# Performance work log

Measured on AMD Instinct MI355X. Metric: run time of the kernel, lower is better.

The kernel has to match this reference:

```python
import jax, jax.numpy as jnp
import numpy as np

A_DIM, HID, D_EMB, K_CODES, N_TOK = 6, 256, 128, 2048, 65536
BETA = 0.25


def _linear_init(k, fan_in, fan_out):
    lim = 1.0 / np.sqrt(fan_in)
    kw, kb = jax.random.split(k)
    W = jax.random.uniform(kw, (fan_in, fan_out), minval=-lim, maxval=lim, dtype=jnp.float32)
    b = jax.random.uniform(kb, (fan_out,), minval=-lim, maxval=lim, dtype=jnp.float32)
    return W, b


def setup_inputs() -> dict:
    key = jax.random.key(0)
    ks = jax.random.split(key, 8)
    action = jax.random.normal(ks[0], (1, N_TOK, A_DIM), dtype=jnp.float32)
    W_e1, b_e1 = _linear_init(ks[1], A_DIM, HID)
    W_e2, b_e2 = _linear_init(ks[2], HID, HID)
    W_e3, b_e3 = _linear_init(ks[3], HID, D_EMB)
    # codebook init: uniform(-1/K, 1/K) as in the torch module
    emb = jax.random.uniform(ks[4], (K_CODES, D_EMB), minval=-1.0 / K_CODES, maxval=1.0 / K_CODES, dtype=jnp.float32)
    W_d1, b_d1 = _linear_init(ks[5], D_EMB, HID)
    W_d2, b_d2 = _linear_init(ks[6], HID, HID)
    W_d3, b_d3 = _linear_init(ks[7], HID, A_DIM)
    return dict(action=action,
                W_e1=W_e1, b_e1=b_e1, W_e2=W_e2, b_e2=b_e2, W_e3=W_e3, b_e3=b_e3,
                emb=emb,
                W_d1=W_d1, b_d1=b_d1, W_d2=W_d2, b_d2=b_d2, W_d3=W_d3, b_d3=b_d3)


def reference(action, W_e1, b_e1, W_e2, b_e2, W_e3, b_e3, emb,
              W_d1, b_d1, W_d2, b_d2, W_d3, b_d3):
    sg = jax.lax.stop_gradient
    # encoder MLP; note original code does encoder(action)[0] -> [N, D]
    h = jax.nn.relu(action @ W_e1 + b_e1)
    h = jax.nn.relu(h @ W_e2 + b_e2)
    enc = (h @ W_e3 + b_e3)[0]                         # [N, D]
    # squared-distance to codebook: [N, K]
    dist = (jnp.sum(enc ** 2, axis=1, keepdims=True)
            + jnp.sum(emb ** 2, axis=1)
            - 2.0 * enc @ emb.T)
    idx = jnp.argmin(dist, axis=1)                     # [N]
    one_hot = jax.nn.one_hot(idx, emb.shape[0], dtype=enc.dtype)  # [N, K]
    q = one_hot @ emb                                  # [N, D]
    commitment_loss = jnp.mean((sg(q) - enc) ** 2)
    embedding_loss = jnp.mean((q - sg(enc)) ** 2)
    vq_loss = BETA * commitment_loss + embedding_loss
    # straight-through estimator
    q_st = enc + sg(q - enc)
    # decoder MLP
    d = jax.nn.relu(q_st @ W_d1 + b_d1)
    d = jax.nn.relu(d @ W_d2 + b_d2)
    recons = jnp.tanh(d @ W_d3 + b_d3)                 # [N, A]
    recons_loss = jnp.mean((recons - action[0]) ** 2)
    total = recons_loss + vq_loss
    return jnp.stack([total, recons_loss, vq_loss])
```

## Files before the change

### kernel.cpp

```cpp
#include <hip/hip_runtime.h>
#include <stdint.h>

typedef unsigned short u16;
typedef float f32x4 __attribute__((ext_vector_type(4)));
typedef short short8 __attribute__((ext_vector_type(8)));
typedef unsigned uint4v __attribute__((ext_vector_type(4)));

enum { NT = 65536, KC = 2048, D = 128, H = 256, A_DIM = 6 };

__device__ __forceinline__ u16 f2bf(float f) {
    union { float f; unsigned u; } x; x.f = f;
    unsigned r = x.u + 0x7FFFu + ((x.u >> 16) & 1u);
    return (u16)(r >> 16);
}
__device__ __forceinline__ float bf2f(u16 u) {
    union { unsigned u; float f; } x; x.u = ((unsigned)u) << 16;
    return x.f;
}

typedef __attribute__((address_space(1))) void gvoid;
typedef __attribute__((address_space(3))) void lvoid;
__device__ __forceinline__ void gload_lds16(const void* g, void* l) {
    __builtin_amdgcn_global_load_lds((gvoid*)g, (lvoid*)l, 16, 0, 0);
}

__global__ void prep(const float* __restrict__ W_e2, const float* __restrict__ W_e3,
                     const float* __restrict__ W_d1, const float* __restrict__ W_d2,
                     const float* __restrict__ emb,
                     u16* __restrict__ We2T, u16* __restrict__ We3T,
                     u16* __restrict__ Wd1T, u16* __restrict__ Wd2T,
                     u16* __restrict__ emb_bf, float* __restrict__ norm2,
                     float* __restrict__ sums) {
    int b = blockIdx.x, t = threadIdx.x;
    if (b == 0 && t < 2) sums[t] = 0.f;
    if (b < 256)       { int e = b * 256 + t;          int i = e >> 8, j = e & 255; We2T[j * 256 + i] = f2bf(W_e2[e]); }
    else if (b < 384)  { int e = (b - 256) * 256 + t;  int i = e >> 7, j = e & 127; We3T[j * 256 + i] = f2bf(W_e3[e]); }
    else if (b < 512)  { int e = (b - 384) * 256 + t;  int i = e >> 8, j = e & 255; Wd1T[j * 128 + i] = f2bf(W_d1[e]); }
    else if (b < 768)  { int e = (b - 512) * 256 + t;  int i = e >> 8, j = e & 255; Wd2T[j * 256 + i] = f2bf(W_d2[e]); }
    else if (b < 1792) { int e = (b - 768) * 256 + t;  emb_bf[e] = f2bf(emb[e]); }
    else {
        int lane = t & 63, w = t >> 6;
        int r = (b - 1792) * 4 + w;
        float v0 = emb[(size_t)r * D + lane];
        float v1 = emb[(size_t)r * D + 64 + lane];
        float s = v0 * v0 + v1 * v1;
#pragma unroll
        for (int off = 32; off; off >>= 1) s += __shfl_xor(s, off);
        if (lane == 0) norm2[r] = s;
    }
}

__global__ __launch_bounds__(256) void enc1(const float* __restrict__ act, const float* __restrict__ W,
                                            const float* __restrict__ b, u16* __restrict__ h1) {
    const int gid = blockIdx.x * 256 + threadIdx.x;
    const int row = gid >> 5;
    const int col0 = (gid & 31) << 3;
    float x[A_DIM];
#pragma unroll
    for (int i = 0; i < A_DIM; i++) x[i] = act[(size_t)row * A_DIM + i];
    float s[8];
#pragma unroll
    for (int c = 0; c < 8; c++) s[c] = b[col0 + c];
#pragma unroll
    for (int i = 0; i < A_DIM; i++) {
        float xi = x[i];
#pragma unroll
        for (int c = 0; c < 8; c++) s[c] = fmaf(xi, W[i * H + col0 + c], s[c]);
    }
    uint4v o;
#pragma unroll
    for (int c2 = 0; c2 < 4; c2++)
        o[c2] = (unsigned)f2bf(fmaxf(s[c2 * 2], 0.f)) | ((unsigned)f2bf(fmaxf(s[c2 * 2 + 1], 0.f)) << 16);
    *(uint4v*)&h1[(size_t)row * H + col0] = o;
}

__global__ __launch_bounds__(256) void enc23_fused(
    const u16* __restrict__ h1g,
    const u16* __restrict__ We2T, const float* __restrict__ b2,
    const u16* __restrict__ We3T, const float* __restrict__ b3,
    u16* __restrict__ encb) {
    __shared__ __align__(16) u16 hA[64 * 256];
    __shared__ __align__(16) u16 sB[256 * 64];
    const int t = threadIdx.x, lane = t & 63, w = t >> 6;
    const int l15 = lane & 15, khalf = lane >> 4;
    const int row0 = blockIdx.x * 64;
#pragma unroll
    for (int p = 0; p < 8; p++) {
        int db = (p * 256 + t) * 16;
        int r = db >> 9;
        int col = ((db & 511) ^ ((r & 7) << 4)) >> 1;
        gload_lds16(h1g + (size_t)(row0 + r) * H + col, (char*)hA + db);
    }
    int sbDst[8], sbRow[8], sbCol[8];
#pragma unroll
    for (int p = 0; p < 8; p++) {
        int db = (p * 256 + t) * 16;
        int r = db >> 7;
        sbDst[p] = db; sbRow[p] = r;
        sbCol[p] = ((db & 127) ^ ((r & 7) << 4)) >> 1;
    }
    const int kbase = khalf * 8;
    f32x4 acc[4][4] = {};
    for (int kst = 0; kst < 4; kst++) {
        if (kst) __syncthreads();
        const int k0 = kst * 64;
#pragma unroll
        for (int p = 0; p < 8; p++)
            gload_lds16(We2T + (size_t)sbRow[p] * H + k0 + sbCol[p], (char*)sB + sbDst[p]);
        __syncthreads();
#pragma unroll
        for (int ks = 0; ks < 2; ks++) {
            const int k = k0 + ks * 32 + kbase;
            const int kb = (ks * 32 + kbase) << 1;
            short8 av[4], bv[4];
#pragma unroll
            for (int m = 0; m < 4; m++) {
                int rA = m * 16 + l15;
                av[m] = *(const short8*)((const char*)hA + ((rA << 9) | ((k << 1) ^ ((rA & 7) << 4))));
            }
#pragma unroll
            for (int n = 0; n < 4; n++) {
                int rB = w * 64 + n * 16 + l15;
                bv[n] = *(const short8*)((const char*)sB + ((rB << 7) | (kb ^ ((rB & 7) << 4))));
            }
#pragma unroll
            for (int m = 0; m < 4; m++)
#pragma unroll
                for (int n = 0; n < 4; n++)
                    acc[m][n] = __builtin_amdgcn_mfma_f32_16x16x32_bf16(av[m], bv[n], acc[m][n], 0, 0, 0);
        }
    }
    __syncthreads();
#pragma unroll
    for (int n = 0; n < 4; n++) {
        int col = w * 64 + n * 16 + l15;
        float bs = b2[col];
#pragma unroll
        for (int m = 0; m < 4; m++)
#pragma unroll
            for (int j = 0; j < 4; j++) {
                int row = m * 16 + khalf * 4 + j;
                float v = fmaxf(acc[m][n][j] + bs, 0.f);
                *(u16*)((char*)hA + ((row << 9) | ((col << 1) ^ ((row & 7) << 4)))) = f2bf(v);
            }
    }
    __syncthreads();
    f32x4 acc2[4][2] = {};
    for (int kst = 0; kst < 4; kst++) {
        if (kst) __syncthreads();
        const int k0 = kst * 64;
#pragma unroll
        for (int p = 0; p < 4; p++)
            gload_lds16(We3T + (size_t)sbRow[p] * H + k0 + sbCol[p], (char*)sB + sbDst[p]);
        __syncthreads();
#pragma unroll
        for (int ks = 0; ks < 2; ks++) {
            const int k = k0 + ks * 32 + kbase;
            const int kb = (ks * 32 + kbase) << 1;
            short8 av[4], bv[2];
#pragma unroll
            for (int m = 0; m < 4; m++) {
                int rA = m * 16 + l15;
                av[m] = *(const short8*)((const char*)hA + ((rA << 9) | ((k << 1) ^ ((rA & 7) << 4))));
            }
#pragma unroll
            for (int n = 0; n < 2; n++) {
                int rB = w * 32 + n * 16 + l15;
                bv[n] = *(const short8*)((const char*)sB + ((rB << 7) | (kb ^ ((rB & 7) << 4))));
            }
#pragma unroll
            for (int m = 0; m < 4; m++)
#pragma unroll
                for (int n = 0; n < 2; n++)
                    acc2[m][n] = __builtin_amdgcn_mfma_f32_16x16x32_bf16(av[m], bv[n], acc2[m][n], 0, 0, 0);
        }
    }
    __syncthreads();
#pragma unroll
    for (int n = 0; n < 2; n++) {
        int col = w * 32 + n * 16 + l15;
        float bs = b3[col];
#pragma unroll
        for (int m = 0; m < 4; m++)
#pragma unroll
            for (int j = 0; j < 4; j++) {
                int row = m * 16 + khalf * 4 + j;
                ((u16*)sB)[row * 128 + col] = f2bf(acc2[m][n][j] + bs);
            }
    }
    __syncthreads();
#pragma unroll
    for (int p = 0; p < 4; p++) {
        int db = (p * 256 + t) * 16;
        *(uint4v*)((char*)(encb + (size_t)row0 * D) + db) = *(const uint4v*)((const char*)sB + db);
    }
}

__global__ __launch_bounds__(256) void dec_fused(
    const u16* __restrict__ qb,
    const u16* __restrict__ Wd1T, const float* __restrict__ bd1,
    const u16* __restrict__ Wd2T, const float* __restrict__ bd2,
    const float* __restrict__ W3, float* __restrict__ part) {
    __shared__ __align__(16) u16 qA[64 * 128];
    __shared__ __align__(16) u16 hA[64 * 256];
    __shared__ __align__(16) u16 sB[256 * 64];
    const int t = threadIdx.x, lane = t & 63, w = t >> 6;
    const int l15 = lane & 15, khalf = lane >> 4;
    const int row0 = blockIdx.x * 64;
#pragma unroll
    for (int p = 0; p < 4; p++) {
        int db = (p * 256 + t) * 16;
        int r = db >> 8;
        int col = ((db & 255) ^ ((r & 7) << 4)) >> 1;
        gload_lds16(qb + (size_t)(row0 + r) * D + col, (char*)qA + db);
    }
    int sbDst[8], sbRow[8], sbCol[8];
#pragma unroll
    for (int p = 0; p < 8; p++) {
        int db = (p * 256 + t) * 16;
        int r = db >> 7;
        sbDst[p] = db; sbRow[p] = r;
        sbCol[p] = ((db & 127) ^ ((r & 7) << 4)) >> 1;
    }
    const int kbase = khalf * 8;
    f32x4 acc[4][4] = {};
    for (int kst = 0; kst < 2; kst++) {
        if (kst) __syncthreads();
        const int k0 = kst * 64;
#pragma unroll
        for (int p = 0; p < 8; p++)
            gload_lds16(Wd1T + (size_t)sbRow[p] * D + k0 + sbCol[p], (char*)sB + sbDst[p]);
        __syncthreads();
#pragma unroll
        for (int ks = 0; ks < 2; ks++) {
            const int k = k0 + ks * 32 + kbase;
            const int kb = (ks * 32 + kbase) << 1;
            short8 av[4], bv[4];
#pragma unroll
            for (int m = 0; m < 4; m++) {
                int rA = m * 16 + l15;
                av[m] = *(const short8*)((const char*)qA + ((rA << 8) | ((k << 1) ^ ((rA & 7) << 4))));
            }
#pragma unroll
            for (int n = 0; n < 4; n++) {
                int rB = w * 64 + n * 16 + l15;
                bv[n] = *(const short8*)((const char*)sB + ((rB << 7) | (kb ^ ((rB & 7) << 4))));
            }
#pragma unroll
            for (int m = 0; m < 4; m++)
#pragma unroll
                for (int n = 0; n < 4; n++)
                    acc[m][n] = __builtin_amdgcn_mfma_f32_16x16x32_bf16(av[m], bv[n], acc[m][n], 0, 0, 0);
        }
    }
#pragma unroll
    for (int n = 0; n < 4; n++) {
        int col = w * 64 + n * 16 + l15;
        float bs = bd1[col];
#pragma unroll
        for (int m = 0; m < 4; m++)
#pragma unroll
            for (int j = 0; j < 4; j++) {
                int row = m * 16 + khalf * 4 + j;
                float v = fmaxf(acc[m][n][j] + bs, 0.f);
                *(u16*)((char*)hA + ((row << 9) | ((col << 1) ^ ((row & 7) << 4)))) = f2bf(v);
            }
    }
    __syncthreads();
    f32x4 acc2[4][4] = {};
    for (int kst = 0; kst < 4; kst++) {
        if (kst) __syncthreads();
        const int k0 = kst * 64;
#pragma unroll
        for (int p = 0; p < 8; p++)
            gload_lds16(Wd2T + (size_t)sbRow[p] * H + k0 + sbCol[p], (char*)sB + sbDst[p]);
        __syncthreads();
#pragma unroll
        for (int ks = 0; ks < 2; ks++) {
            const int k = k0 + ks * 32 + kbase;
            const int kb = (ks * 32 + kbase) << 1;
            short8 av[4], bv[4];
#pragma unroll
            for (int m = 0; m < 4; m++) {
                int rA = m * 16 + l15;
                av[m] = *(const short8*)((const char*)hA + ((rA << 9) | ((k << 1) ^ ((rA & 7) << 4))));
            }
#pragma unroll
            for (int n = 0; n < 4; n++) {
                int rB = w * 64 + n * 16 + l15;
                bv[n] = *(const short8*)((const char*)sB + ((rB << 7) | (kb ^ ((rB & 7) << 4))));
            }
#pragma unroll
            for (int m = 0; m < 4; m++)
#pragma unroll
                for (int n = 0; n < 4; n++)
                    acc2[m][n] = __builtin_amdgcn_mfma_f32_16x16x32_bf16(av[m], bv[n], acc2[m][n], 0, 0, 0);
        }
    }
    float W3r[4][A_DIM], bs[4];
#pragma unroll
    for (int n = 0; n < 4; n++) {
        int col = w * 64 + n * 16 + l15;
        bs[n] = bd2[col];
#pragma unroll
        for (int j = 0; j < A_DIM; j++) W3r[n][j] = W3[col * A_DIM + j];
    }
    float* ps = part + (size_t)w * NT * A_DIM;
#pragma unroll
    for (int m = 0; m < 4; m++) {
#pragma unroll
        for (int j = 0; j < 4; j++) {
            int row = row0 + m * 16 + khalf * 4 + j;
            float p6[A_DIM] = {};
#pragma unroll
            for (int n = 0; n < 4; n++) {
                float v = fmaxf(acc2[m][n][j] + bs[n], 0.f);
#pragma unroll
                for (int jj = 0; jj < A_DIM; jj++) p6[jj] = fmaf(v, W3r[n][jj], p6[jj]);
            }
#pragma unroll
            for (int off = 1; off < 16; off <<= 1)
#pragma unroll
                for (int jj = 0; jj < A_DIM; jj++) p6[jj] += __shfl_xor(p6[jj], off);
            if (l15 == 0) {
#pragma unroll
                for (int jj = 0; jj < A_DIM; jj++) ps[(size_t)row * A_DIM + jj] = p6[jj];
            }
        }
    }
}

__global__ __launch_bounds__(256) void head_final(const float* __restrict__ part, const float* __restrict__ b3,
                                                  const float* __restrict__ act, float* __restrict__ sums) {
    __shared__ float sred[4];
    const int t = threadIdx.x, lane = t & 63, w = t >> 6;
    const int n = blockIdx.x * 256 + t;
    float s = 0.f;
#pragma unroll
    for (int j = 0; j < A_DIM; j++) {
        float v = b3[j];
#pragma unroll
        for (int sl = 0; sl < 4; sl++) v += part[(size_t)sl * NT * A_DIM + (size_t)n * A_DIM + j];
        float r = tanhf(v);
        float df = r - act[(size_t)n * A_DIM + j];
        s += df * df;
    }
#pragma unroll
    for (int off = 32; off; off >>= 1) s += __shfl_xor(s, off);
    if (lane == 0) sred[w] = s;
    __syncthreads();
    if (t == 0) atomicAdd(&sums[1], sred[0] + sred[1] + sred[2] + sred[3]);
}

__global__ __launch_bounds__(256) void vq_dist(const u16* __restrict__ enc_bf, const u16* __restrict__ emb_bf,
                                               const float* __restrict__ emb, const float* __restrict__ norm2,
                                               u16* __restrict__ q_bf, float* __restrict__ sums) {
    __shared__ u16 sA[128 * 128];
    __shared__ u16 sB[128 * 128];
    __shared__ float sN[KC];
    __shared__ unsigned sKey[128];
    __shared__ float svq[4];
    const int t = threadIdx.x, lane = t & 63, w = t >> 6, wr = w >> 1, wc = w & 1;
    const int row0 = blockIdx.x * 128;
    int srow[8], sdst[8], scol[8];
#pragma unroll
    for (int p = 0; p < 8; p++) {
        int db = (p * 256 + t) * 16;
        int row = db >> 8;
        srow[p] = row; sdst[p] = db;
        scol[p] = ((db & 255) ^ ((row & 7) << 4)) >> 1;
    }
#pragma unroll
    for (int p = 0; p < 8; p++) gload_lds16(enc_bf + (size_t)(row0 + srow[p]) * D + scol[p], (char*)sA + sdst[p]);
#pragma unroll
    for (int p = 0; p < 8; p++) gload_lds16(emb_bf + (size_t)srow[p] * D + scol[p], (char*)sB + sdst[p]);
    for (int i = t; i < KC; i += 256) sN[i] = norm2[i] + 1.0f;
    const int ra = wr * 64 + (lane & 15), rb = wc * 64 + (lane & 15);
    const int kbase = (lane >> 4) * 8;
    int boff[4][4];
#pragma unroll
    for (int m = 0; m < 4; m++)
#pragma unroll
        for (int ks = 0; ks < 4; ks++) {
            int rB = rb + m * 16;
            int kb = (ks * 32 + kbase) << 1;
            boff[m][ks] = (rB << 8) | (kb ^ ((rB & 7) << 4));
        }
    __syncthreads();
    short8 av[4][4];
#pragma unroll
    for (int m = 0; m < 4; m++)
#pragma unroll
        for (int ks = 0; ks < 4; ks++) {
            int rA = ra + m * 16;
            int kb = (ks * 32 + kbase) << 1;
            av[m][ks] = *(const short8*)((const char*)sA + ((rA << 8) | (kb ^ ((rA & 7) << 4))));
        }
    unsigned minKey[4][4];
#pragma unroll
    for (int m = 0; m < 4; m++)
#pragma unroll
        for (int j = 0; j < 4; j++) minKey[m][j] = 0xFFFFFFFFu;
    for (int ch = 0; ch < 16; ch++) {
        if (ch) {
            __syncthreads();
            const u16* src = emb_bf + (size_t)ch * 128 * D;
#pragma unroll
            for (int p = 0; p < 8; p++) gload_lds16(src + (size_t)srow[p] * D + scol[p], (char*)sB + sdst[p]);
            __syncthreads();
        }
        f32x4 acc[4][4] = {};
#pragma unroll
        for (int ks = 0; ks < 4; ks++) {
            short8 bv[4];
#pragma unroll
            for (int n = 0; n < 4; n++) bv[n] = *(const short8*)((const char*)sB + boff[n][ks]);
#pragma unroll
            for (int m = 0; m < 4; m++)
#pragma unroll
                for (int n = 0; n < 4; n++)
                    acc[m][n] = __builtin_amdgcn_mfma_f32_16x16x32_bf16(av[m][ks], bv[n], acc[m][n], 0, 0, 0);
        }
#pragma unroll
        for (int n = 0; n < 4; n++) {
            int k = ch * 128 + rb + n * 16;
            float nn = sN[k];
#pragma unroll
            for (int m = 0; m < 4; m++)
#pragma unroll
                for (int j = 0; j < 4; j++) {
                    float c = fmaf(acc[m][n][j], -2.f, nn);
                    unsigned key = (__float_as_uint(c) & 0xFFFFF800u) | (unsigned)k;
                    minKey[m][j] = min(minKey[m][j], key);
                }
        }
    }
#pragma unroll
    for (int off = 1; off < 16; off <<= 1) {
#pragma unroll
        for (int m = 0; m < 4; m++)
#pragma unroll
            for (int j = 0; j < 4; j++)
                minKey[m][j] = min(minKey[m][j], (unsigned)__shfl_xor((int)minKey[m][j], off));
    }
    __syncthreads();
    if (wc == 0 && (lane & 15) == 0) {
#pragma unroll
        for (int m = 0; m < 4; m++)
#pragma unroll
            for (int j = 0; j < 4; j++) {
                int row = wr * 64 + m * 16 + (lane >> 4) * 4 + j;
                sKey[row] = minKey[m][j];
            }
    }
    __syncthreads();
    if (wc == 1 && (lane & 15) == 0) {
#pragma unroll
        for (int m = 0; m < 4; m++)
#pragma unroll
            for (int j = 0; j < 4; j++) {
                int row = wr * 64 + m * 16 + (lane >> 4) * 4 + j;
                if (minKey[m][j] < sKey[row]) sKey[row] = minKey[m][j];
            }
    }
    __syncthreads();
    float vql = 0.f;
    for (int rr = 0; rr < 32; rr++) {
        int row = w * 32 + rr;
        int k = (int)(sKey[row] & 0x7FFu);
        float q0 = emb[(size_t)k * D + lane];
        float q1 = emb[(size_t)k * D + 64 + lane];
        int swz = (row & 7) << 4;
        float e0 = bf2f(*(const u16*)((const char*)sA + ((row << 8) | ((lane << 1) ^ swz))));
        float e1 = bf2f(*(const u16*)((const char*)sA + ((row << 8) | (((lane + 64) << 1) ^ swz))));
        float d0 = q0 - e0, d1 = q1 - e1;
        vql += d0 * d0 + d1 * d1;
        q_bf[(size_t)(row0 + row) * D + lane] = f2bf(q0);
        q_bf[(size_t)(row0 + row) * D + 64 + lane] = f2bf(q1);
    }
#pragma unroll
    for (int off = 32; off; off >>= 1) vql += __shfl_xor(vql, off);
    if (lane == 0) svq[w] = vql;
    __syncthreads();
    if (t == 0) atomicAdd(&sums[0], svq[0] + svq[1] + svq[2] + svq[3]);
}

__global__ void finalize(const float* __restrict__ sums, float* __restrict__ out) {
    if (threadIdx.x == 0) {
        float vq = 1.25f * sums[0] / (float)(NT * D);
        float rec = sums[1] / (float)(NT * A_DIM);
        out[0] = rec + vq;
        out[1] = rec;
        out[2] = vq;
    }
}

extern "C" void kernel_launch(void* const* d_in, const int* in_sizes, int n_in,
                              void* d_out, int out_size, void* d_ws, size_t ws_size,
                              hipStream_t stream) {
    const float* action = (const float*)d_in[0];
    const float* W_e1 = (const float*)d_in[1];
    const float* b_e1 = (const float*)d_in[2];
    const float* W_e2 = (const float*)d_in[3];
    const float* b_e2 = (const float*)d_in[4];
    const float* W_e3 = (const float*)d_in[5];
    const float* b_e3 = (const float*)d_in[6];
    const float* emb  = (const float*)d_in[7];
    const float* W_d1 = (const float*)d_in[8];
    const float* b_d1 = (const float*)d_in[9];
    const float* W_d2 = (const float*)d_in[10];
    const float* b_d2 = (const float*)d_in[11];
    const float* W_d3 = (const float*)d_in[12];
    const float* b_d3 = (const float*)d_in[13];

    char* ws = (char*)d_ws;
    float* sums  = (float*)ws;
    float* norm2 = (float*)(ws + 256);
    u16* We2T   = (u16*)(ws + 8448);
    u16* We3T   = (u16*)(ws + 139520);
    u16* Wd1T   = (u16*)(ws + 205056);
    u16* Wd2T   = (u16*)(ws + 270592);
    u16* emb_bf = (u16*)(ws + 401664);
    u16* h1     = (u16*)(ws + 925952);
    float* part = (float*)(ws + 925952 + 33554432);
    u16* encb   = (u16*)(ws + 925952 + 67108864);
    u16* qb     = (u16*)(ws + 925952 + 83886080);

    prep<<<2304, 256, 0, stream>>>(W_e2, W_e3, W_d1, W_d2, emb, We2T, We3T, Wd1T, Wd2T, emb_bf, norm2, sums);
    enc1<<<NT * 32 / 256, 256, 0, stream>>>(action, W_e1, b_e1, h1);
    enc23_fused<<<NT / 64, 256, 0, stream>>>(h1, We2T, b_e2, We3T, b_e3, encb);
    vq_dist<<<NT / 128, 256, 0, stream>>>(encb, emb_bf, emb, norm2, qb, sums);
    dec_fused<<<NT / 64, 256, 0, stream>>>(qb, Wd1T, b_d1, Wd2T, b_d2, W_d3, part);
    head_final<<<NT / 256, 256, 0, stream>>>(part, b_d3, action, sums);
    finalize<<<1, 64, 0, stream>>>(sums, (float*)d_out);
}
```

Before: 148.3 us.

## Pass code indices instead of quantized vectors; gather codebook rows in decoder

vq_dist now writes one int index per token instead of a bf16 quantized row, and dec_fused gathers the codebook rows directly from emb_bf through the indices. The VQ loss is rebuilt algebraically as the min distance key value plus the sum of enc squared, avoiding a per-row fp32 codebook gather. This cuts the 16MB quantized-vector write and read, at the cost of an extra sync and index load in the decoder. The loss now relies on the packed distance key's truncated precision and an assumed offset of 1.0, which may change numerics slightly.

After: 157.1 us. 1.06x slower.

```diff
diff --git a/kernel.cpp b/kernel.cpp
--- a/kernel.cpp
+++ b/kernel.cpp
@@ -197,22 +197,25 @@
 }
 
 __global__ __launch_bounds__(256) void dec_fused(
-    const u16* __restrict__ qb,
+    const u16* __restrict__ emb_bf, const int* __restrict__ idxbuf,
     const u16* __restrict__ Wd1T, const float* __restrict__ bd1,
     const u16* __restrict__ Wd2T, const float* __restrict__ bd2,
     const float* __restrict__ W3, float* __restrict__ part) {
     __shared__ __align__(16) u16 qA[64 * 128];
     __shared__ __align__(16) u16 hA[64 * 256];
     __shared__ __align__(16) u16 sB[256 * 64];
+    __shared__ int sIdxL[64];
     const int t = threadIdx.x, lane = t & 63, w = t >> 6;
     const int l15 = lane & 15, khalf = lane >> 4;
     const int row0 = blockIdx.x * 64;
+    if (t < 64) sIdxL[t] = idxbuf[row0 + t];
+    __syncthreads();
 #pragma unroll
     for (int p = 0; p < 4; p++) {
         int db = (p * 256 + t) * 16;
         int r = db >> 8;
         int col = ((db & 255) ^ ((r & 7) << 4)) >> 1;
-        gload_lds16(qb + (size_t)(row0 + r) * D + col, (char*)qA + db);
+        gload_lds16(emb_bf + (size_t)sIdxL[r] * D + col, (char*)qA + db);
     }
     int sbDst[8], sbRow[8], sbCol[8];
 #pragma unroll
@@ -353,8 +356,8 @@
 }
 
 __global__ __launch_bounds__(256) void vq_dist(const u16* __restrict__ enc_bf, const u16* __restrict__ emb_bf,
-                                               const float* __restrict__ emb, const float* __restrict__ norm2,
-                                               u16* __restrict__ q_bf, float* __restrict__ sums) {
+                                               const float* __restrict__ norm2,
+                                               int* __restrict__ idxbuf, float* __restrict__ sums) {
     __shared__ u16 sA[128 * 128];
     __shared__ u16 sB[128 * 128];
     __shared__ float sN[KC];
@@ -465,18 +468,16 @@
     }
     __syncthreads();
     float vql = 0.f;
-    for (int rr = 0; rr < 32; rr++) {
-        int row = w * 32 + rr;
-        int k = (int)(sKey[row] & 0x7FFu);
-        float q0 = emb[(size_t)k * D + lane];
-        float q1 = emb[(size_t)k * D + 64 + lane];
-        int swz = (row & 7) << 4;
-        float e0 = bf2f(*(const u16*)((const char*)sA + ((row << 8) | ((lane << 1) ^ swz))));
-        float e1 = bf2f(*(const u16*)((const char*)sA + ((row << 8) | (((lane + 64) << 1) ^ swz))));
-        float d0 = q0 - e0, d1 = q1 - e1;
-        vql += d0 * d0 + d1 * d1;
-        q_bf[(size_t)(row0 + row) * D + lane] = f2bf(q0);
-        q_bf[(size_t)(row0 + row) * D + 64 + lane] = f2bf(q1);
+    if (t < 128) {
+        unsigned sk = sKey[t];
+        idxbuf[row0 + t] = (int)(sk & 0x7FFu);
+        vql = __uint_as_float(sk & 0xFFFFF800u) - 1.0f;
+    }
+#pragma unroll
+    for (int i = 0; i < 8; i++) {
+        short8 v = *(const short8*)((const char*)sA + i * 4096 + t * 16);
+#pragma unroll
+        for (int j = 0; j < 8; j++) { float e = bf2f((u16)v[j]); vql = fmaf(e, e, vql); }
     }
 #pragma unroll
     for (int off = 32; off; off >>= 1) vql += __shfl_xor(vql, off);
@@ -524,13 +525,13 @@
     u16* h1     = (u16*)(ws + 925952);
     float* part = (float*)(ws + 925952 + 33554432);
     u16* encb   = (u16*)(ws + 925952 + 67108864);
-    u16* qb     = (u16*)(ws + 925952 + 83886080);
+    int* idxbuf = (int*)(ws + 925952 + 83886080);
 
     prep<<<2304, 256, 0, stream>>>(W_e2, W_e3, W_d1, W_d2, emb, We2T, We3T, Wd1T, Wd2T, emb_bf, norm2, sums);
     enc1<<<NT * 32 / 256, 256, 0, stream>>>(action, W_e1, b_e1, h1);
     enc23_fused<<<NT / 64, 256, 0, stream>>>(h1, We2T, b_e2, We3T, b_e3, encb);
-    vq_dist<<<NT / 128, 256, 0, stream>>>(encb, emb_bf, emb, norm2, qb, sums);
-    dec_fused<<<NT / 64, 256, 0, stream>>>(qb, Wd1T, b_d1, Wd2T, b_d2, W_d3, part);
+    vq_dist<<<NT / 128, 256, 0, stream>>>(encb, emb_bf, norm2, idxbuf, sums);
+    dec_fused<<<NT / 64, 256, 0, stream>>>(emb_bf, idxbuf, Wd1T, b_d1, Wd2T, b_d2, W_d3, part);
     head_final<<<NT / 256, 256, 0, stream>>>(part, b_d3, action, sums);
     finalize<<<1, 64, 0, stream>>>(sums, (float*)d_out);
 }
```
